# Performance work log

Hardware: AMD Instinct MI355X
Metric: run time of the kernel (lower is better)

The kernel has to match this reference:

```python
import jax, jax.numpy as jnp
import numpy as np

NEG_SLOPE = 0.01  # torch leaky_relu default

def _lrelu(x):
    return jax.nn.leaky_relu(x, NEG_SLOPE)

def _l2norm(x, axis):
    # torch F.normalize(p=2, eps=1e-12)
    n = jnp.linalg.norm(x, axis=axis, keepdims=True)
    return x / jnp.maximum(n, 1e-12)

def setup_inputs() -> dict:
    key = jax.random.key(0)
    ks = jax.random.split(key, 12)
    Nda, Nq, C, Din, Dout = 10000, 64, 1024, 128, 256
    target_adj = (jax.random.uniform(ks[0], (Nda, Nda)) < 0.002).astype(jnp.float32)
    query_adj = (jax.random.uniform(ks[1], (Nq, Nq)) < 0.2).astype(jnp.float32)
    node_features_da = jax.random.normal(ks[2], (Nda, Din), dtype=jnp.float32)
    node_features_q = jax.random.normal(ks[3], (Nq, Din), dtype=jnp.float32)
    candidate_set = jax.random.randint(ks[4], (C,), 0, Nda)
    candidate_adj = (jax.random.uniform(ks[5], (C, C)) < 0.01).astype(jnp.float32)
    s_in = 1.0 / np.sqrt(Din).astype(np.float32)
    s_out = 1.0 / np.sqrt(Dout).astype(np.float32)
    W1_da = jax.random.normal(ks[6], (Din, Dout), dtype=jnp.float32) * s_in
    W1_q = jax.random.normal(ks[7], (Din, Dout), dtype=jnp.float32) * s_in
    W2_da = jax.random.normal(ks[8], (Dout, Dout), dtype=jnp.float32) * s_out
    W2_q = jax.random.normal(ks[9], (Dout, Dout), dtype=jnp.float32) * s_out
    threshold = jnp.float32(0.2)
    return {"target_adj": target_adj, "node_features_da": node_features_da,
            "query_adj": query_adj, "node_features_q": node_features_q,
            "candidate_set": candidate_set, "candidate_adj": candidate_adj,
            "threshold": threshold, "W1_da": W1_da, "W1_q": W1_q,
            "W2_da": W2_da, "W2_q": W2_q}

def _cross_cosine(q, da, candidate_set):
    # cosine similarity between each query node and each candidate target node: [Nq, C]
    return _l2norm(q, 1) @ _l2norm(da[candidate_set], 1).T

def reference(target_adj, node_features_da, query_adj, node_features_q,
              candidate_set, candidate_adj, threshold, W1_da, W1_q, W2_da, W2_q):
    # layer 1: GCN propagation on both graphs (gcn(adj,x) = adj @ x @ W)
    da1 = _lrelu(target_adj @ (node_features_da @ W1_da))   # [Nda, D]
    q1 = _lrelu(query_adj @ (node_features_q @ W1_q))       # [Nq, D]
    c1 = _cross_cosine(q1, da1, candidate_set)               # [Nq, C]
    pre_da1 = da1[candidate_set]                             # [C, D]
    # NOTE: da1[candidate_set].data = ... mutates a temporary in torch -> no-op on da1
    att_da1 = _lrelu(da1)                                    # dropout in eval = identity
    h1_q = c1 @ pre_da1                                      # [Nq, D]
    att_q1 = _lrelu(q1 + _l2norm(h1_q, 0))
    # layer 2
    da2 = _lrelu(target_adj @ (att_da1 @ W2_da))
    q2 = _lrelu(query_adj @ (att_q1 @ W2_q))
    c2 = _cross_cosine(q2, da2, candidate_set)
    pre_da2 = da2[candidate_set]
    att_da2 = _lrelu(da2)                                    # in-place update is again a no-op
    h2_q = c2 @ pre_da2
    att_q2 = _lrelu(q2 + _l2norm(h2_q, 0))
    # graph-level matching score per target node
    emb = jnp.mean(att_q2, axis=0, keepdims=True)            # [1, D]
    num = att_da2 @ emb[0]                                   # [Nda]
    den = jnp.maximum(jnp.linalg.norm(att_da2, axis=1) * jnp.linalg.norm(emb), 1e-8)
    end = (num / den)[None, :]                               # [1, Nda]
    # threshold selection expressed with a mask (jit-safe, same math: excluded
    # rows/cols are zero and do not affect L2 norms, sums, or the trace)
    m = (end[0] > threshold).astype(att_da2.dtype)           # [Nda]
    F_ = att_da2 * m[:, None]
    re_adj = F_ @ F_.T                                       # [Nda, Nda]
    nor_re = _l2norm(re_adj, 1) * target_adj                 # elementwise with original adj
    cnt = jnp.sum(m)
    total = jnp.sum(nor_re)
    tr = jnp.trace(nor_re)
    has = cnt > 0
    pre_avg_degree = jnp.where(has, total / jnp.maximum(cnt, 1.0), 0.0)
    pre_avg_nodes = jnp.where(has, tr, 0.0)
    pre_density = jnp.where(has, 2.0 * total / (tr * (tr - 1.0) + 1e-4), 0.0)
    return (end, att_da2, att_q2, pre_avg_degree, pre_density, pre_avg_nodes)
```

## Files before the change

kernel.cpp:

```cpp
#include <hip/hip_runtime.h>

constexpr int NDA = 10000;
constexpr int NQ  = 64;
constexpr int CND = 1024;
constexpr int DIN = 128;
constexpr int D   = 256;
constexpr int CAP = 96;

#define LRELU(x) ((x) >= 0.f ? (x) : 0.01f * (x))

__device__ __forceinline__ float wave_red64(float v) {
#pragma unroll
    for (int o = 32; o; o >>= 1) v += __shfl_down(v, o);
    return v;
}

__global__ __launch_bounds__(256) void build_csr(const float* __restrict__ adj,
                                                 int* __restrict__ cols,
                                                 int* __restrict__ rowcnt) {
    int row = blockIdx.x;
    __shared__ int scnt;
    if (threadIdx.x == 0) scnt = 0;
    __syncthreads();
    const float4* rp = (const float4*)(adj + (size_t)row * NDA);
    for (int i = threadIdx.x; i < NDA / 4; i += 256) {
        float4 v = rp[i];
        if (v.x != 0.f) { int s = atomicAdd(&scnt, 1); if (s < CAP) cols[row * CAP + s] = 4 * i; }
        if (v.y != 0.f) { int s = atomicAdd(&scnt, 1); if (s < CAP) cols[row * CAP + s] = 4 * i + 1; }
        if (v.z != 0.f) { int s = atomicAdd(&scnt, 1); if (s < CAP) cols[row * CAP + s] = 4 * i + 2; }
        if (v.w != 0.f) { int s = atomicAdd(&scnt, 1); if (s < CAP) cols[row * CAP + s] = 4 * i + 3; }
    }
    __syncthreads();
    if (threadIdx.x == 0) rowcnt[row] = min(scnt, CAP);
}

template <bool RELU_A, bool RELU_C>
__global__ __launch_bounds__(256) void gemm64(const float* __restrict__ A,
                                              const float* __restrict__ B,
                                              float* __restrict__ C,
                                              int M, int N, int K) {
    __shared__ float As[16][68];
    __shared__ float Bs[16][68];
    const int bm = blockIdx.x * 64;
    const int bn = blockIdx.y * 64;
    const int tid = threadIdx.x;
    const int tx = tid & 15, ty = tid >> 4;
    float acc[4][4] = {};
    for (int k0 = 0; k0 < K; k0 += 16) {
        {
            int m = tid >> 2;
            int k4 = (tid & 3) * 4;
            float4 v = make_float4(0.f, 0.f, 0.f, 0.f);
            if (bm + m < M) v = *(const float4*)(A + (size_t)(bm + m) * K + k0 + k4);
            if (RELU_A) { v.x = LRELU(v.x); v.y = LRELU(v.y); v.z = LRELU(v.z); v.w = LRELU(v.w); }
            As[k4 + 0][m] = v.x; As[k4 + 1][m] = v.y; As[k4 + 2][m] = v.z; As[k4 + 3][m] = v.w;
        }
        {
            int kk = tid >> 4;
            int n4 = (tid & 15) * 4;
            float4 v = *(const float4*)(B + (size_t)(k0 + kk) * N + bn + n4);
            Bs[kk][n4 + 0] = v.x; Bs[kk][n4 + 1] = v.y; Bs[kk][n4 + 2] = v.z; Bs[kk][n4 + 3] = v.w;
        }
        __syncthreads();
#pragma unroll
        for (int kk = 0; kk < 16; kk++) {
            float av[4], bv[4];
#pragma unroll
            for (int i = 0; i < 4; i++) av[i] = As[kk][ty * 4 + i];
#pragma unroll
            for (int j = 0; j < 4; j++) bv[j] = Bs[kk][tx * 4 + j];
#pragma unroll
            for (int i = 0; i < 4; i++)
#pragma unroll
                for (int j = 0; j < 4; j++) acc[i][j] += av[i] * bv[j];
        }
        __syncthreads();
    }
#pragma unroll
    for (int i = 0; i < 4; i++) {
        int r = bm + ty * 4 + i;
        if (r < M) {
            float4 v;
            v.x = acc[i][0]; v.y = acc[i][1]; v.z = acc[i][2]; v.w = acc[i][3];
            if (RELU_C) { v.x = LRELU(v.x); v.y = LRELU(v.y); v.z = LRELU(v.z); v.w = LRELU(v.w); }
            *(float4*)(C + (size_t)r * N + bn + tx * 4) = v;
        }
    }
}

__global__ __launch_bounds__(256) void spmm_csr(const int* __restrict__ cols,
                                                const int* __restrict__ rowcnt,
                                                const float* __restrict__ X,
                                                float* __restrict__ out1,
                                                float* __restrict__ out2) {
    int row = blockIdx.x;
    int d = threadIdx.x;
    int cnt = rowcnt[row];
    __shared__ int sc[CAP];
    if (d < cnt) sc[d] = cols[row * CAP + d];
    __syncthreads();
    float a0 = 0.f, a1 = 0.f, a2 = 0.f, a3 = 0.f;
    int k = 0;
    for (; k + 4 <= cnt; k += 4) {
        a0 += X[(size_t)sc[k + 0] * D + d];
        a1 += X[(size_t)sc[k + 1] * D + d];
        a2 += X[(size_t)sc[k + 2] * D + d];
        a3 += X[(size_t)sc[k + 3] * D + d];
    }
    for (; k < cnt; k++) a0 += X[(size_t)sc[k] * D + d];
    float v = LRELU(a0 + a1 + a2 + a3);
    out1[(size_t)row * D + d] = v;
    if (out2) out2[(size_t)row * D + d] = LRELU(v);
}

__global__ __launch_bounds__(256) void rownorms_kernel(const float* __restrict__ da,
                                                       const int* __restrict__ cand,
                                                       float* __restrict__ rnc,
                                                       const float* __restrict__ q,
                                                       float* __restrict__ rnq) {
    int b = blockIdx.x;
    const float* src;
    float* dst;
    if (b < CND) { src = da + (size_t)cand[b] * D; dst = rnc + b; }
    else         { src = q + (size_t)(b - CND) * D; dst = rnq + (b - CND); }
    float v = src[threadIdx.x];
    float p = wave_red64(v * v);
    __shared__ float red[4];
    int w = threadIdx.x >> 6, lane = threadIdx.x & 63;
    if (lane == 0) red[w] = p;
    __syncthreads();
    if (threadIdx.x == 0) *dst = sqrtf(red[0] + red[1] + red[2] + red[3]);
}

__global__ __launch_bounds__(256) void cosmat_kernel(const float* __restrict__ q,
                                                     const float* __restrict__ rnq,
                                                     const float* __restrict__ da,
                                                     const int* __restrict__ cand,
                                                     const float* __restrict__ rnc,
                                                     float* __restrict__ cm) {
    __shared__ float qs[D];
    int r = blockIdx.x;
    int cc = blockIdx.y * 256 + threadIdx.x;
    qs[threadIdx.x] = q[r * D + threadIdx.x];
    __syncthreads();
    int row = cand[cc];
    const float4* ap = (const float4*)(da + (size_t)row * D);
    float dot = 0.f;
#pragma unroll 8
    for (int k = 0; k < D / 4; k++) {
        float4 v = ap[k];
        dot += qs[4 * k] * v.x + qs[4 * k + 1] * v.y + qs[4 * k + 2] * v.z + qs[4 * k + 3] * v.w;
    }
    float denom = fmaxf(rnq[r], 1e-12f) * fmaxf(rnc[cc], 1e-12f);
    cm[r * CND + cc] = dot / denom;
}

__global__ __launch_bounds__(256) void hq_kernel(const float* __restrict__ cm,
                                                 const float* __restrict__ da,
                                                 const int* __restrict__ cand,
                                                 float* __restrict__ h) {
    __shared__ float swt[CND];
    __shared__ int sci[CND];
    int r = blockIdx.x, d = threadIdx.x;
    for (int s = 0; s < CND / 256; s++) {
        swt[s * 256 + d] = cm[r * CND + s * 256 + d];
        sci[s * 256 + d] = cand[s * 256 + d];
    }
    __syncthreads();
    float a0 = 0.f, a1 = 0.f, a2 = 0.f, a3 = 0.f, a4 = 0.f, a5 = 0.f, a6 = 0.f, a7 = 0.f;
    for (int c = 0; c < CND; c += 8) {
        a0 += swt[c + 0] * da[(size_t)sci[c + 0] * D + d];
        a1 += swt[c + 1] * da[(size_t)sci[c + 1] * D + d];
        a2 += swt[c + 2] * da[(size_t)sci[c + 2] * D + d];
        a3 += swt[c + 3] * da[(size_t)sci[c + 3] * D + d];
        a4 += swt[c + 4] * da[(size_t)sci[c + 4] * D + d];
        a5 += swt[c + 5] * da[(size_t)sci[c + 5] * D + d];
        a6 += swt[c + 6] * da[(size_t)sci[c + 6] * D + d];
        a7 += swt[c + 7] * da[(size_t)sci[c + 7] * D + d];
    }
    h[r * D + d] = ((a0 + a1) + (a2 + a3)) + ((a4 + a5) + (a6 + a7));
}

__global__ __launch_bounds__(256) void attq_kernel(const float* __restrict__ q,
                                                   const float* __restrict__ h,
                                                   float* __restrict__ attq,
                                                   float* __restrict__ emb) {
    int d = threadIdx.x;
    float hv[NQ];
    float ss = 0.f;
#pragma unroll
    for (int r = 0; r < NQ; r++) {
        hv[r] = h[r * D + d];
        ss += hv[r] * hv[r];
    }
    float inv = 1.f / fmaxf(sqrtf(ss), 1e-12f);
    float es = 0.f;
#pragma unroll
    for (int r = 0; r < NQ; r++) {
        float v = q[r * D + d] + hv[r] * inv;
        v = LRELU(v);
        attq[r * D + d] = v;
        es += v;
    }
    if (emb) {
        float e = es * (1.f / (float)NQ);
        emb[d] = e;
        float p = wave_red64(e * e);
        __shared__ float red[4];
        int w = d >> 6, lane = d & 63;
        if (lane == 0) red[w] = p;
        __syncthreads();
        if (d == 0) emb[D] = sqrtf(red[0] + red[1] + red[2] + red[3]);
    }
}

__global__ __launch_bounds__(256) void end_kernel(const float* __restrict__ A,
                                                  const float* __restrict__ emb,
                                                  const float* __restrict__ thr_p,
                                                  float* __restrict__ endv,
                                                  float* __restrict__ m,
                                                  float* __restrict__ cnt) {
    __shared__ float se[D];
    __shared__ float scnt;
    int d = threadIdx.x;
    se[d] = emb[d];
    if (d == 0) scnt = 0.f;
    __syncthreads();
    float embn = emb[D];
    float thr = *thr_p;
    int w = d >> 6, lane = d & 63;
    int row = blockIdx.x * 4 + w;
    const float* ar = A + (size_t)row * D;
    float num = 0.f, sq = 0.f;
#pragma unroll
    for (int s = 0; s < 4; s++) {
        float v = ar[lane + 64 * s];
        num += v * se[lane + 64 * s];
        sq += v * v;
    }
#pragma unroll
    for (int o = 32; o; o >>= 1) { num += __shfl_down(num, o); sq += __shfl_down(sq, o); }
    if (lane == 0) {
        float den = fmaxf(sqrtf(sq) * embn, 1e-8f);
        float e = num / den;
        endv[row] = e;
        float mv = e > thr ? 1.f : 0.f;
        m[row] = mv;
        if (mv != 0.f) atomicAdd(&scnt, 1.f);
    }
    __syncthreads();
    if (d == 0 && scnt != 0.f) atomicAdd(cnt, scnt);
}

constexpr int GCHUNK = 400;
__global__ __launch_bounds__(256) void G_kernel(const float* __restrict__ A,
                                                const float* __restrict__ m,
                                                float* __restrict__ G) {
    __shared__ float SA[8][64], SB[8][64];
    int ti = blockIdx.x >> 2, tj = blockIdx.x & 3;
    int base = blockIdx.y * GCHUNK;
    int tid = threadIdx.x;
    int tx = tid & 15, ty = tid >> 4;
    float acc[4][4] = {};
    for (int g0 = 0; g0 < GCHUNK; g0 += 8) {
        for (int l = tid; l < 512; l += 256) {
            int rr = l >> 6, c = l & 63;
            int r = base + g0 + rr;
            float mv = m[r];
            SA[rr][c] = A[(size_t)r * D + ti * 64 + c] * mv;
            SB[rr][c] = A[(size_t)r * D + tj * 64 + c];
        }
        __syncthreads();
#pragma unroll
        for (int rr = 0; rr < 8; rr++) {
            float av[4], bv[4];
#pragma unroll
            for (int i = 0; i < 4; i++) av[i] = SA[rr][ty * 4 + i];
#pragma unroll
            for (int j = 0; j < 4; j++) bv[j] = SB[rr][tx * 4 + j];
#pragma unroll
            for (int i = 0; i < 4; i++)
#pragma unroll
                for (int j = 0; j < 4; j++) acc[i][j] += av[i] * bv[j];
        }
        __syncthreads();
    }
#pragma unroll
    for (int i = 0; i < 4; i++)
#pragma unroll
        for (int j = 0; j < 4; j++)
            atomicAdd(&G[(ti * 64 + ty * 4 + i) * D + tj * 64 + tx * 4 + j], acc[i][j]);
}

__global__ __launch_bounds__(256) void final_kernel(const int* __restrict__ cols,
                                                    const int* __restrict__ rowcnt,
                                                    const float* __restrict__ m,
                                                    const float* __restrict__ A,
                                                    const float* __restrict__ H,
                                                    double* __restrict__ total,
                                                    double* __restrict__ tr) {
    int i = blockIdx.x;
    if (m[i] == 0.f) return;
    __shared__ float sa[D];
    __shared__ int sc[CAP];
    __shared__ float red[4], red2[4];
    __shared__ float sdenom;
    int d = threadIdx.x;
    float av = A[(size_t)i * D + d];
    sa[d] = av;
    int cnt = rowcnt[i];
    if (d < cnt) sc[d] = cols[i * CAP + d];
    float p = wave_red64(av * H[(size_t)i * D + d]);
    int w = d >> 6, lane = d & 63;
    if (lane == 0) red[w] = p;
    __syncthreads();
    if (d == 0) sdenom = fmaxf(sqrtf(red[0] + red[1] + red[2] + red[3]), 1e-12f);
    __syncthreads();
    float accs = 0.f, acct = 0.f;
    for (int k = w; k < cnt; k += 4) {
        int j = sc[k];
        if (m[j] != 0.f) {
            const float* aj = A + (size_t)j * D;
            float t = sa[lane] * aj[lane] + sa[lane + 64] * aj[lane + 64]
                    + sa[lane + 128] * aj[lane + 128] + sa[lane + 192] * aj[lane + 192];
            t = wave_red64(t);
            if (lane == 0) { accs += t; if (j == i) acct += t; }
        }
    }
    if (lane == 0) { red[w] = accs; red2[w] = acct; }
    __syncthreads();
    if (d == 0) {
        float s = red[0] + red[1] + red[2] + red[3];
        float t2 = red2[0] + red2[1] + red2[2] + red2[3];
        double inv = 1.0 / (double)sdenom;
        if (s != 0.f) atomicAdd(total, (double)s * inv);
        if (t2 != 0.f) atomicAdd(tr, (double)t2 * inv);
    }
}

__global__ void scalars_kernel(const float* __restrict__ cnt,
                               const double* __restrict__ total,
                               const double* __restrict__ tr,
                               float* __restrict__ out) {
    float c = *cnt;
    float T = (float)*total;
    float R = (float)*tr;
    bool has = c > 0.f;
    out[0] = has ? (T / fmaxf(c, 1.f)) : 0.f;
    out[1] = has ? (2.f * T / (R * (R - 1.f) + 1e-4f)) : 0.f;
    out[2] = has ? R : 0.f;
}

extern "C" void kernel_launch(void* const* d_in, const int* in_sizes, int n_in,
                              void* d_out, int out_size, void* d_ws, size_t ws_size,
                              hipStream_t stream) {
    (void)in_sizes; (void)n_in; (void)out_size; (void)ws_size;
    const float* adj  = (const float*)d_in[0];
    const float* Fda  = (const float*)d_in[1];
    const float* Qadj = (const float*)d_in[2];
    const float* Fq   = (const float*)d_in[3];
    const int*   cand = (const int*)d_in[4];
    const float* thr  = (const float*)d_in[6];
    const float* W1da = (const float*)d_in[7];
    const float* W1q  = (const float*)d_in[8];
    const float* W2da = (const float*)d_in[9];
    const float* W2q  = (const float*)d_in[10];

    float* out = (float*)d_out;
    float* o_end    = out;
    float* o_attda2 = out + NDA;
    float* o_attq2  = out + NDA + (size_t)NDA * D;
    float* o_sc     = o_attq2 + NQ * D;

    char* w = (char*)d_ws;
    size_t off = 0;
    auto alloc = [&](size_t b) { size_t r = off; off += (b + 255) & ~(size_t)255; return r; };
    float* bufA = (float*)(w + alloc((size_t)NDA * D * 4));
    float* bufB = (float*)(w + alloc((size_t)NDA * D * 4));
    float* bufC = (float*)(w + alloc((size_t)NDA * D * 4));
    int* colsb   = (int*)(w + alloc((size_t)NDA * CAP * 4));
    int* rowcntb = (int*)(w + alloc((size_t)NDA * 4));
    float* mbuf  = (float*)(w + alloc((size_t)NDA * 4));
    char* zbase = w + alloc(262144 + 256);
    float* Gb    = (float*)zbase;
    float* cntb  = (float*)(zbase + 262144);
    double* totb = (double*)(zbase + 262144 + 8);
    double* trb  = (double*)(zbase + 262144 + 16);
    float* xq   = (float*)(w + alloc((size_t)NQ * D * 4));
    float* q1b  = (float*)(w + alloc((size_t)NQ * D * 4));
    float* aq1  = (float*)(w + alloc((size_t)NQ * D * 4));
    float* q2b  = (float*)(w + alloc((size_t)NQ * D * 4));
    float* hb   = (float*)(w + alloc((size_t)NQ * D * 4));
    float* cm   = (float*)(w + alloc((size_t)NQ * CND * 4));
    float* rnc  = (float*)(w + alloc((size_t)CND * 4));
    float* rnq  = (float*)(w + alloc((size_t)NQ * 4));
    float* embb = (float*)(w + alloc((size_t)(D + 1) * 4));

    hipMemsetAsync(zbase, 0, 262144 + 256, stream);

    const dim3 gBig((NDA + 63) / 64, D / 64);
    const dim3 gSmall(1, D / 64);

    gemm64<false, false><<<gBig, 256, 0, stream>>>(Fda, W1da, bufA, NDA, D, DIN);
    build_csr<<<NDA, 256, 0, stream>>>(adj, colsb, rowcntb);
    gemm64<false, false><<<gSmall, 256, 0, stream>>>(Fq, W1q, xq, NQ, D, DIN);
    gemm64<false, true><<<gSmall, 256, 0, stream>>>(Qadj, xq, q1b, NQ, D, NQ);
    spmm_csr<<<NDA, 256, 0, stream>>>(colsb, rowcntb, bufA, bufB, (float*)nullptr);
    rownorms_kernel<<<CND + NQ, 256, 0, stream>>>(bufB, cand, rnc, q1b, rnq);
    cosmat_kernel<<<dim3(NQ, CND / 256), 256, 0, stream>>>(q1b, rnq, bufB, cand, rnc, cm);
    hq_kernel<<<NQ, 256, 0, stream>>>(cm, bufB, cand, hb);
    attq_kernel<<<1, 256, 0, stream>>>(q1b, hb, aq1, (float*)nullptr);
    gemm64<true, false><<<gBig, 256, 0, stream>>>(bufB, W2da, bufA, NDA, D, D);
    gemm64<false, false><<<gSmall, 256, 0, stream>>>(aq1, W2q, xq, NQ, D, D);
    gemm64<false, true><<<gSmall, 256, 0, stream>>>(Qadj, xq, q2b, NQ, D, NQ);
    spmm_csr<<<NDA, 256, 0, stream>>>(colsb, rowcntb, bufA, bufC, o_attda2);
    rownorms_kernel<<<CND + NQ, 256, 0, stream>>>(bufC, cand, rnc, q2b, rnq);
    cosmat_kernel<<<dim3(NQ, CND / 256), 256, 0, stream>>>(q2b, rnq, bufC, cand, rnc, cm);
    hq_kernel<<<NQ, 256, 0, stream>>>(cm, bufC, cand, hb);
    attq_kernel<<<1, 256, 0, stream>>>(q2b, hb, o_attq2, embb);
    end_kernel<<<NDA / 4, 256, 0, stream>>>(o_attda2, embb, thr, o_end, mbuf, cntb);
    G_kernel<<<dim3(16, NDA / GCHUNK), 256, 0, stream>>>(o_attda2, mbuf, Gb);
    gemm64<false, false><<<gBig, 256, 0, stream>>>(o_attda2, Gb, bufB, NDA, D, D);
    final_kernel<<<NDA, 256, 0, stream>>>(colsb, rowcntb, mbuf, o_attda2, bufB, totb, trb);
    scalars_kernel<<<1, 1, 0, stream>>>(cntb, totb, trb, o_sc);
}
```

Measured before the change: 1.028 ms.

## Merge independent stages into combined launches and fuse cosine-similarity with aggregation

New measurement: 1.050 ms. 2.1% more time.

```diff
diff --git a/kernel.cpp b/kernel.cpp
--- a/kernel.cpp
+++ b/kernel.cpp
@@ -6,6 +6,7 @@
 constexpr int DIN = 128;
 constexpr int D   = 256;
 constexpr int CAP = 96;
+constexpr int NB_BIG = ((NDA + 63) / 64) * (D / 64);
 
 #define LRELU(x) ((x) >= 0.f ? (x) : 0.01f * (x))
 
@@ -15,10 +16,76 @@
     return v;
 }
 
-__global__ __launch_bounds__(256) void build_csr(const float* __restrict__ adj,
-                                                 int* __restrict__ cols,
-                                                 int* __restrict__ rowcnt) {
-    int row = blockIdx.x;
+struct GemmSmem { float As[32][68]; float Bs[32][68]; };
+
+template <bool RELU_A, bool RELU_C>
+__device__ __forceinline__ void gemm_body(GemmSmem& sm, int bx, int by,
+                                          const float* __restrict__ A,
+                                          const float* __restrict__ B,
+                                          float* __restrict__ C,
+                                          int M, int N, int K) {
+    const int bm = bx * 64, bn = by * 64;
+    const int tid = threadIdx.x;
+    const int tx = tid & 15, ty = tid >> 4;
+    const int lm = tid >> 2, lk = (tid & 3) * 8;
+    const int kb = tid >> 3, nb = (tid & 7) * 8;
+    const bool aValid = (bm + lm) < M;
+    const float* aPtr = A + (size_t)(bm + lm) * K + lk;
+    const float* bPtr = B + (size_t)kb * N + bn + nb;
+    float4 ra0 = make_float4(0.f, 0.f, 0.f, 0.f), ra1 = ra0, rb0, rb1;
+    if (aValid) { ra0 = *(const float4*)aPtr; ra1 = *(const float4*)(aPtr + 4); }
+    rb0 = *(const float4*)bPtr;
+    rb1 = *(const float4*)(bPtr + 4);
+    float acc[4][4] = {};
+    for (int k0 = 0; k0 < K; k0 += 32) {
+        float4 wa0 = ra0, wa1 = ra1, wb0 = rb0, wb1 = rb1;
+        if (RELU_A) {
+            wa0.x = LRELU(wa0.x); wa0.y = LRELU(wa0.y); wa0.z = LRELU(wa0.z); wa0.w = LRELU(wa0.w);
+            wa1.x = LRELU(wa1.x); wa1.y = LRELU(wa1.y); wa1.z = LRELU(wa1.z); wa1.w = LRELU(wa1.w);
+        }
+        sm.As[lk + 0][lm] = wa0.x; sm.As[lk + 1][lm] = wa0.y;
+        sm.As[lk + 2][lm] = wa0.z; sm.As[lk + 3][lm] = wa0.w;
+        sm.As[lk + 4][lm] = wa1.x; sm.As[lk + 5][lm] = wa1.y;
+        sm.As[lk + 6][lm] = wa1.z; sm.As[lk + 7][lm] = wa1.w;
+        *(float4*)&sm.Bs[kb][nb]     = wb0;
+        *(float4*)&sm.Bs[kb][nb + 4] = wb1;
+        __syncthreads();
+        if (k0 + 32 < K) {
+            if (aValid) {
+                ra0 = *(const float4*)(aPtr + k0 + 32);
+                ra1 = *(const float4*)(aPtr + k0 + 36);
+            }
+            rb0 = *(const float4*)(bPtr + (size_t)(k0 + 32) * N);
+            rb1 = *(const float4*)(bPtr + (size_t)(k0 + 32) * N + 4);
+        }
+#pragma unroll
+        for (int kk = 0; kk < 32; kk++) {
+            float av[4], bv[4];
+#pragma unroll
+            for (int i = 0; i < 4; i++) av[i] = sm.As[kk][ty * 4 + i];
+#pragma unroll
+            for (int j = 0; j < 4; j++) bv[j] = sm.Bs[kk][tx * 4 + j];
+#pragma unroll
+            for (int i = 0; i < 4; i++)
+#pragma unroll
+                for (int j = 0; j < 4; j++) acc[i][j] += av[i] * bv[j];
+        }
+        __syncthreads();
+    }
+#pragma unroll
+    for (int i = 0; i < 4; i++) {
+        int r = bm + ty * 4 + i;
+        if (r < M) {
+            float4 v = make_float4(acc[i][0], acc[i][1], acc[i][2], acc[i][3]);
+            if (RELU_C) { v.x = LRELU(v.x); v.y = LRELU(v.y); v.z = LRELU(v.z); v.w = LRELU(v.w); }
+            *(float4*)(C + (size_t)r * N + bn + tx * 4) = v;
+        }
+    }
+}
+
+__device__ __forceinline__ void csr_body(const float* __restrict__ adj,
+                                         int* __restrict__ cols,
+                                         int* __restrict__ rowcnt, int row) {
     __shared__ int scnt;
     if (threadIdx.x == 0) scnt = 0;
     __syncthreads();
@@ -34,66 +101,11 @@
     if (threadIdx.x == 0) rowcnt[row] = min(scnt, CAP);
 }
 
-template <bool RELU_A, bool RELU_C>
-__global__ __launch_bounds__(256) void gemm64(const float* __restrict__ A,
-                                              const float* __restrict__ B,
-                                              float* __restrict__ C,
-                                              int M, int N, int K) {
-    __shared__ float As[16][68];
-    __shared__ float Bs[16][68];
-    const int bm = blockIdx.x * 64;
-    const int bn = blockIdx.y * 64;
-    const int tid = threadIdx.x;
-    const int tx = tid & 15, ty = tid >> 4;
-    float acc[4][4] = {};
-    for (int k0 = 0; k0 < K; k0 += 16) {
-        {
-            int m = tid >> 2;
-            int k4 = (tid & 3) * 4;
-            float4 v = make_float4(0.f, 0.f, 0.f, 0.f);
-            if (bm + m < M) v = *(const float4*)(A + (size_t)(bm + m) * K + k0 + k4);
-            if (RELU_A) { v.x = LRELU(v.x); v.y = LRELU(v.y); v.z = LRELU(v.z); v.w = LRELU(v.w); }
-            As[k4 + 0][m] = v.x; As[k4 + 1][m] = v.y; As[k4 + 2][m] = v.z; As[k4 + 3][m] = v.w;
-        }
-        {
-            int kk = tid >> 4;
-            int n4 = (tid & 15) * 4;
-            float4 v = *(const float4*)(B + (size_t)(k0 + kk) * N + bn + n4);
-            Bs[kk][n4 + 0] = v.x; Bs[kk][n4 + 1] = v.y; Bs[kk][n4 + 2] = v.z; Bs[kk][n4 + 3] = v.w;
-        }
-        __syncthreads();
-#pragma unroll
-        for (int kk = 0; kk < 16; kk++) {
-            float av[4], bv[4];
-#pragma unroll
-            for (int i = 0; i < 4; i++) av[i] = As[kk][ty * 4 + i];
-#pragma unroll
-            for (int j = 0; j < 4; j++) bv[j] = Bs[kk][tx * 4 + j];
-#pragma unroll
-            for (int i = 0; i < 4; i++)
-#pragma unroll
-                for (int j = 0; j < 4; j++) acc[i][j] += av[i] * bv[j];
-        }
-        __syncthreads();
-    }
-#pragma unroll
-    for (int i = 0; i < 4; i++) {
-        int r = bm + ty * 4 + i;
-        if (r < M) {
-            float4 v;
-            v.x = acc[i][0]; v.y = acc[i][1]; v.z = acc[i][2]; v.w = acc[i][3];
-            if (RELU_C) { v.x = LRELU(v.x); v.y = LRELU(v.y); v.z = LRELU(v.z); v.w = LRELU(v.w); }
-            *(float4*)(C + (size_t)r * N + bn + tx * 4) = v;
-        }
-    }
-}
-
-__global__ __launch_bounds__(256) void spmm_csr(const int* __restrict__ cols,
-                                                const int* __restrict__ rowcnt,
-                                                const float* __restrict__ X,
-                                                float* __restrict__ out1,
-                                                float* __restrict__ out2) {
-    int row = blockIdx.x;
+__device__ __forceinline__ void spmm_body(const int* __restrict__ cols,
+                                          const int* __restrict__ rowcnt,
+                                          const float* __restrict__ X,
+                                          float* __restrict__ out1,
+                                          float* __restrict__ out2, int row) {
     int d = threadIdx.x;
     int cnt = rowcnt[row];
     __shared__ int sc[CAP];
@@ -113,76 +125,114 @@
     if (out2) out2[(size_t)row * D + d] = LRELU(v);
 }
 
-__global__ __launch_bounds__(256) void rownorms_kernel(const float* __restrict__ da,
-                                                       const int* __restrict__ cand,
-                                                       float* __restrict__ rnc,
-                                                       const float* __restrict__ q,
-                                                       float* __restrict__ rnq) {
-    int b = blockIdx.x;
-    const float* src;
-    float* dst;
-    if (b < CND) { src = da + (size_t)cand[b] * D; dst = rnc + b; }
-    else         { src = q + (size_t)(b - CND) * D; dst = rnq + (b - CND); }
-    float v = src[threadIdx.x];
-    float p = wave_red64(v * v);
+__global__ __launch_bounds__(256) void stage0_kernel(const float* __restrict__ adj,
+                                                     int* __restrict__ cols,
+                                                     int* __restrict__ rowcnt,
+                                                     const float* __restrict__ Fda,
+                                                     const float* __restrict__ W1da,
+                                                     float* __restrict__ X1,
+                                                     const float* __restrict__ Fq,
+                                                     const float* __restrict__ W1q,
+                                                     float* __restrict__ Xq) {
+    __shared__ GemmSmem gs;
+    int bid = blockIdx.x;
+    if (bid < NB_BIG) {
+        gemm_body<false, false>(gs, bid >> 2, bid & 3, Fda, W1da, X1, NDA, D, DIN);
+    } else if (bid < NB_BIG + 4) {
+        gemm_body<false, false>(gs, 0, bid - NB_BIG, Fq, W1q, Xq, NQ, D, DIN);
+    } else {
+        csr_body(adj, cols, rowcnt, bid - (NB_BIG + 4));
+    }
+}
+
+__global__ __launch_bounds__(256) void stage_sg_kernel(const int* __restrict__ cols,
+                                                       const int* __restrict__ rowcnt,
+                                                       const float* __restrict__ X,
+                                                       float* __restrict__ out1,
+                                                       float* __restrict__ out2,
+                                                       const float* __restrict__ Aq,
+                                                       const float* __restrict__ Bq,
+                                                       float* __restrict__ Cq) {
+    __shared__ GemmSmem gs;
+    int bid = blockIdx.x;
+    if (bid < 4) {
+        gemm_body<false, true>(gs, 0, bid, Aq, Bq, Cq, NQ, D, NQ);
+    } else {
+        spmm_body(cols, rowcnt, X, out1, out2, bid - 4);
+    }
+}
+
+__global__ __launch_bounds__(256) void stage4_kernel(const float* __restrict__ da1,
+                                                     const float* __restrict__ W2da,
+                                                     float* __restrict__ Y2,
+                                                     const float* __restrict__ aq1,
+                                                     const float* __restrict__ W2q,
+                                                     float* __restrict__ Zq) {
+    __shared__ GemmSmem gs;
+    int bid = blockIdx.x;
+    if (bid < NB_BIG) {
+        gemm_body<true, false>(gs, bid >> 2, bid & 3, da1, W2da, Y2, NDA, D, D);
+    } else {
+        gemm_body<false, false>(gs, 0, bid - NB_BIG, aq1, W2q, Zq, NQ, D, D);
+    }
+}
+
+__global__ __launch_bounds__(256) void gemmH_kernel(const float* __restrict__ A,
+                                                    const float* __restrict__ B,
+                                                    float* __restrict__ C) {
+    __shared__ GemmSmem gs;
+    gemm_body<false, false>(gs, blockIdx.x, blockIdx.y, A, B, C, NDA, D, D);
+}
+
+__global__ __launch_bounds__(256) void cross_kernel(const float* __restrict__ q,
+                                                    const float* __restrict__ da,
+                                                    const int* __restrict__ cand,
+                                                    float* __restrict__ hpart) {
+    __shared__ float qs[D];
+    __shared__ float cmw[256];
+    __shared__ int sci[256];
     __shared__ float red[4];
-    int w = threadIdx.x >> 6, lane = threadIdx.x & 63;
+    __shared__ float sqn;
+    int r = blockIdx.x, qr = blockIdx.y;
+    int d = threadIdx.x;
+    float qv = q[r * D + d];
+    qs[d] = qv;
+    sci[d] = cand[qr * 256 + d];
+    float p = wave_red64(qv * qv);
+    int w = d >> 6, lane = d & 63;
     if (lane == 0) red[w] = p;
     __syncthreads();
-    if (threadIdx.x == 0) *dst = sqrtf(red[0] + red[1] + red[2] + red[3]);
-}
-
-__global__ __launch_bounds__(256) void cosmat_kernel(const float* __restrict__ q,
-                                                     const float* __restrict__ rnq,
-                                                     const float* __restrict__ da,
-                                                     const int* __restrict__ cand,
-                                                     const float* __restrict__ rnc,
-                                                     float* __restrict__ cm) {
-    __shared__ float qs[D];
-    int r = blockIdx.x;
-    int cc = blockIdx.y * 256 + threadIdx.x;
-    qs[threadIdx.x] = q[r * D + threadIdx.x];
-    __syncthreads();
-    int row = cand[cc];
-    const float4* ap = (const float4*)(da + (size_t)row * D);
-    float dot = 0.f;
+    if (d == 0) sqn = fmaxf(sqrtf(red[0] + red[1] + red[2] + red[3]), 1e-12f);
+    __syncthreads();
+    float qn = sqn;
+    {
+        const float4* ap = (const float4*)(da + (size_t)sci[d] * D);
+        float dot = 0.f, sq = 0.f;
 #pragma unroll 8
-    for (int k = 0; k < D / 4; k++) {
-        float4 v = ap[k];
-        dot += qs[4 * k] * v.x + qs[4 * k + 1] * v.y + qs[4 * k + 2] * v.z + qs[4 * k + 3] * v.w;
-    }
-    float denom = fmaxf(rnq[r], 1e-12f) * fmaxf(rnc[cc], 1e-12f);
-    cm[r * CND + cc] = dot / denom;
-}
-
-__global__ __launch_bounds__(256) void hq_kernel(const float* __restrict__ cm,
-                                                 const float* __restrict__ da,
-                                                 const int* __restrict__ cand,
-                                                 float* __restrict__ h) {
-    __shared__ float swt[CND];
-    __shared__ int sci[CND];
-    int r = blockIdx.x, d = threadIdx.x;
-    for (int s = 0; s < CND / 256; s++) {
-        swt[s * 256 + d] = cm[r * CND + s * 256 + d];
-        sci[s * 256 + d] = cand[s * 256 + d];
+        for (int k = 0; k < D / 4; k++) {
+            float4 v = ap[k];
+            dot += qs[4 * k] * v.x + qs[4 * k + 1] * v.y + qs[4 * k + 2] * v.z + qs[4 * k + 3] * v.w;
+            sq  += v.x * v.x + v.y * v.y + v.z * v.z + v.w * v.w;
+        }
+        cmw[d] = dot / (qn * fmaxf(sqrtf(sq), 1e-12f));
     }
     __syncthreads();
     float a0 = 0.f, a1 = 0.f, a2 = 0.f, a3 = 0.f, a4 = 0.f, a5 = 0.f, a6 = 0.f, a7 = 0.f;
-    for (int c = 0; c < CND; c += 8) {
-        a0 += swt[c + 0] * da[(size_t)sci[c + 0] * D + d];
-        a1 += swt[c + 1] * da[(size_t)sci[c + 1] * D + d];
-        a2 += swt[c + 2] * da[(size_t)sci[c + 2] * D + d];
-        a3 += swt[c + 3] * da[(size_t)sci[c + 3] * D + d];
-        a4 += swt[c + 4] * da[(size_t)sci[c + 4] * D + d];
-        a5 += swt[c + 5] * da[(size_t)sci[c + 5] * D + d];
-        a6 += swt[c + 6] * da[(size_t)sci[c + 6] * D + d];
-        a7 += swt[c + 7] * da[(size_t)sci[c + 7] * D + d];
-    }
-    h[r * D + d] = ((a0 + a1) + (a2 + a3)) + ((a4 + a5) + (a6 + a7));
+    for (int c = 0; c < 256; c += 8) {
+        a0 += cmw[c + 0] * da[(size_t)sci[c + 0] * D + d];
+        a1 += cmw[c + 1] * da[(size_t)sci[c + 1] * D + d];
+        a2 += cmw[c + 2] * da[(size_t)sci[c + 2] * D + d];
+        a3 += cmw[c + 3] * da[(size_t)sci[c + 3] * D + d];
+        a4 += cmw[c + 4] * da[(size_t)sci[c + 4] * D + d];
+        a5 += cmw[c + 5] * da[(size_t)sci[c + 5] * D + d];
+        a6 += cmw[c + 6] * da[(size_t)sci[c + 6] * D + d];
+        a7 += cmw[c + 7] * da[(size_t)sci[c + 7] * D + d];
+    }
+    hpart[((size_t)qr * NQ + r) * D + d] = ((a0 + a1) + (a2 + a3)) + ((a4 + a5) + (a6 + a7));
 }
 
 __global__ __launch_bounds__(256) void attq_kernel(const float* __restrict__ q,
-                                                   const float* __restrict__ h,
+                                                   const float* __restrict__ hpart,
                                                    float* __restrict__ attq,
                                                    float* __restrict__ emb) {
     int d = threadIdx.x;
@@ -190,8 +240,12 @@
     float ss = 0.f;
 #pragma unroll
     for (int r = 0; r < NQ; r++) {
-        hv[r] = h[r * D + d];
-        ss += hv[r] * hv[r];
+        float h = hpart[(size_t)r * D + d]
+                + hpart[(size_t)(NQ + r) * D + d]
+                + hpart[(size_t)(2 * NQ + r) * D + d]
+                + hpart[(size_t)(3 * NQ + r) * D + d];
+        hv[r] = h;
+        ss += h * h;
     }
     float inv = 1.f / fmaxf(sqrtf(ss), 1e-12f);
     float es = 0.f;
@@ -301,40 +355,43 @@
                                                     double* __restrict__ tr) {
     int i = blockIdx.x;
     if (m[i] == 0.f) return;
-    __shared__ float sa[D];
+    int d = threadIdx.x;
+    int cnt = rowcnt[i];
     __shared__ int sc[CAP];
-    __shared__ float red[4], red2[4];
-    __shared__ float sdenom;
-    int d = threadIdx.x;
+    __shared__ float smask[CAP];
+    __shared__ int sdiag;
+    __shared__ float r1[4], r2[4], r3[4];
+    if (d == 0) sdiag = 0;
+    if (d < cnt) {
+        int j = cols[i * CAP + d];
+        sc[d] = j;
+        smask[d] = m[j];
+        if (j == i) sdiag = 1;
+    }
+    __syncthreads();
     float av = A[(size_t)i * D + d];
-    sa[d] = av;
-    int cnt = rowcnt[i];
-    if (d < cnt) sc[d] = cols[i * CAP + d];
-    float p = wave_red64(av * H[(size_t)i * D + d]);
+    float hv = H[(size_t)i * D + d];
+    float sd = 0.f;
+    for (int k = 0; k < cnt; k++)
+        if (smask[k] != 0.f) sd += A[(size_t)sc[k] * D + d];
+    float p1 = av * sd, p2 = av * hv, p3 = av * av;
+#pragma unroll
+    for (int o = 32; o; o >>= 1) {
+        p1 += __shfl_down(p1, o);
+        p2 += __shfl_down(p2, o);
+        p3 += __shfl_down(p3, o);
+    }
     int w = d >> 6, lane = d & 63;
-    if (lane == 0) red[w] = p;
-    __syncthreads();
-    if (d == 0) sdenom = fmaxf(sqrtf(red[0] + red[1] + red[2] + red[3]), 1e-12f);
-    __syncthreads();
-    float accs = 0.f, acct = 0.f;
-    for (int k = w; k < cnt; k += 4) {
-        int j = sc[k];
-        if (m[j] != 0.f) {
-            const float* aj = A + (size_t)j * D;
-            float t = sa[lane] * aj[lane] + sa[lane + 64] * aj[lane + 64]
-                    + sa[lane + 128] * aj[lane + 128] + sa[lane + 192] * aj[lane + 192];
-            t = wave_red64(t);
-            if (lane == 0) { accs += t; if (j == i) acct += t; }
-        }
-    }
-    if (lane == 0) { red[w] = accs; red2[w] = acct; }
+    if (lane == 0) { r1[w] = p1; r2[w] = p2; r3[w] = p3; }
     __syncthreads();
     if (d == 0) {
-        float s = red[0] + red[1] + red[2] + red[3];
-        float t2 = red2[0] + red2[1] + red2[2] + red2[3];
-        double inv = 1.0 / (double)sdenom;
-        if (s != 0.f) atomicAdd(total, (double)s * inv);
-        if (t2 != 0.f) atomicAdd(tr, (double)t2 * inv);
+        float num  = r1[0] + r1[1] + r1[2] + r1[3];
+        float den2 = r2[0] + r2[1] + r2[2] + r2[3];
+        float self = r3[0] + r3[1] + r3[2] + r3[3];
+        float denom = fmaxf(sqrtf(den2), 1e-12f);
+        double inv = 1.0 / (double)denom;
+        if (num != 0.f) atomicAdd(total, (double)num * inv);
+        if (sdiag) atomicAdd(tr, (double)self * inv);
     }
 }
 
@@ -390,37 +447,26 @@
     float* q1b  = (float*)(w + alloc((size_t)NQ * D * 4));
     float* aq1  = (float*)(w + alloc((size_t)NQ * D * 4));
     float* q2b  = (float*)(w + alloc((size_t)NQ * D * 4));
-    float* hb   = (float*)(w + alloc((size_t)NQ * D * 4));
-    float* cm   = (float*)(w + alloc((size_t)NQ * CND * 4));
-    float* rnc  = (float*)(w + alloc((size_t)CND * 4));
-    float* rnq  = (float*)(w + alloc((size_t)NQ * 4));
+    float* hpart = (float*)(w + alloc((size_t)4 * NQ * D * 4));
     float* embb = (float*)(w + alloc((size_t)(D + 1) * 4));
 
     hipMemsetAsync(zbase, 0, 262144 + 256, stream);
 
-    const dim3 gBig((NDA + 63) / 64, D / 64);
-    const dim3 gSmall(1, D / 64);
-
-    gemm64<false, false><<<gBig, 256, 0, stream>>>(Fda, W1da, bufA, NDA, D, DIN);
-    build_csr<<<NDA, 256, 0, stream>>>(adj, colsb, rowcntb);
-    gemm64<false, false><<<gSmall, 256, 0, stream>>>(Fq, W1q, xq, NQ, D, DIN);
-    gemm64<false, true><<<gSmall, 256, 0, stream>>>(Qadj, xq, q1b, NQ, D, NQ);
-    spmm_csr<<<NDA, 256, 0, stream>>>(colsb, rowcntb, bufA, bufB, (float*)nullptr);
-    rownorms_kernel<<<CND + NQ, 256, 0, stream>>>(bufB, cand, rnc, q1b, rnq);
-    cosmat_kernel<<<dim3(NQ, CND / 256), 256, 0, stream>>>(q1b, rnq, bufB, cand, rnc, cm);
-    hq_kernel<<<NQ, 256, 0, stream>>>(cm, bufB, cand, hb);
-    attq_kernel<<<1, 256, 0, stream>>>(q1b, hb, aq1, (float*)nullptr);
-    gemm64<true, false><<<gBig, 256, 0, stream>>>(bufB, W2da, bufA, NDA, D, D);
-    gemm64<false, false><<<gSmall, 256, 0, stream>>>(aq1, W2q, xq, NQ, D, D);
-    gemm64<false, true><<<gSmall, 256, 0, stream>>>(Qadj, xq, q2b, NQ, D, NQ);
-    spmm_csr<<<NDA, 256, 0, stream>>>(colsb, rowcntb, bufA, bufC, o_attda2);
-    rownorms_kernel<<<CND + NQ, 256, 0, stream>>>(bufC, cand, rnc, q2b, rnq);
-    cosmat_kernel<<<dim3(NQ, CND / 256), 256, 0, stream>>>(q2b, rnq, bufC, cand, rnc, cm);
-    hq_kernel<<<NQ, 256, 0, stream>>>(cm, bufC, cand, hb);
-    attq_kernel<<<1, 256, 0, stream>>>(q2b, hb, o_attq2, embb);
+    stage0_kernel<<<NB_BIG + 4 + NDA, 256, 0, stream>>>(adj, colsb, rowcntb,
+                                                        Fda, W1da, bufA,
+                                                        Fq, W1q, xq);
+    stage_sg_kernel<<<NDA + 4, 256, 0, stream>>>(colsb, rowcntb, bufA, bufB, (float*)nullptr,
+                                                 Qadj, xq, q1b);
+    cross_kernel<<<dim3(NQ, 4), 256, 0, stream>>>(q1b, bufB, cand, hpart);
+    attq_kernel<<<1, 256, 0, stream>>>(q1b, hpart, aq1, (float*)nullptr);
+    stage4_kernel<<<NB_BIG + 4, 256, 0, stream>>>(bufB, W2da, bufA, aq1, W2q, xq);
+    stage_sg_kernel<<<NDA + 4, 256, 0, stream>>>(colsb, rowcntb, bufA, bufC, o_attda2,
+                                                 Qadj, xq, q2b);
+    cross_kernel<<<dim3(NQ, 4), 256, 0, stream>>>(q2b, bufC, cand, hpart);
+    attq_kernel<<<1, 256, 0, stream>>>(q2b, hpart, o_attq2, embb);
     end_kernel<<<NDA / 4, 256, 0, stream>>>(o_attda2, embb, thr, o_end, mbuf, cntb);
     G_kernel<<<dim3(16, NDA / GCHUNK), 256, 0, stream>>>(o_attda2, mbuf, Gb);
-    gemm64<false, false><<<gBig, 256, 0, stream>>>(o_attda2, Gb, bufB, NDA, D, D);
+    gemmH_kernel<<<dim3((NDA + 63) / 64, D / 64), 256, 0, stream>>>(o_attda2, Gb, bufB);
     final_kernel<<<NDA, 256, 0, stream>>>(colsb, rowcntb, mbuf, o_attda2, bufB, totb, trb);
     scalars_kernel<<<1, 1, 0, stream>>>(cntb, totb, trb, o_sc);
 }
```
